# Kernel tuning notes

Measured on AMD Instinct MI355X. Metric: run time of the kernel, lower is better.

The kernel has to match this reference:

```python
import jax, jax.numpy as jnp
import numpy as np

B = 8192; L = 50; D_EMB = 128
N_USER = 100000; N_MOVIE = 50000; N_DENSE = 8
D = 2 * D_EMB + D_EMB + N_DENSE  # 392 total_input_dim
E = 4; T = 2; H1 = 256; H2 = 128; ATT_H = 64; N_CROSS = 3


def setup_inputs() -> dict:
    key = jax.random.key(0)
    ks = jax.random.split(key, 28)
    rn = lambda k, shape, s=0.02: jax.random.normal(k, shape, jnp.float32) * s
    inp = {
        'userId': jax.random.randint(ks[0], (B,), 0, N_USER),
        'movieId': jax.random.randint(ks[1], (B,), 0, N_MOVIE),
        'seq_history': jax.random.randint(ks[2], (B, L), 0, N_MOVIE),
        'dense_feats': jax.random.normal(ks[3], (B, N_DENSE), jnp.float32),
        # embeddings (row 0 is padding_idx -> zeros)
        'emb_user': rn(ks[4], (N_USER + 1, D_EMB)).at[0].set(0.0),
        'emb_movie': rn(ks[5], (N_MOVIE + 1, D_EMB)).at[0].set(0.0),
        # DIN attention MLP: input [q,k,q-k,q*k] = 4*D_EMB
        'att_w1': rn(ks[6], (4 * D_EMB, ATT_H)), 'att_b1': jnp.zeros((ATT_H,), jnp.float32),
        'att_w2': rn(ks[7], (ATT_H, 1)), 'att_b2': jnp.zeros((1,), jnp.float32),
        # LayerNorms
        'in_gamma': jnp.ones((D,), jnp.float32), 'in_beta': jnp.zeros((D,), jnp.float32),
        'cr_gamma': jnp.ones((D,), jnp.float32), 'cr_beta': jnp.zeros((D,), jnp.float32),
        # CrossNetV2: x_{l+1} = x0 * (x_l W_l + b_l) + x_l
        'cross_W': rn(ks[8], (N_CROSS, D, D)), 'cross_b': jnp.zeros((N_CROSS, D), jnp.float32),
        # MMoE experts: Linear(D,H1)-ReLU-Linear(H1,H2), batched over E
        'exp_w1': rn(ks[9], (E, D, H1)), 'exp_b1': jnp.zeros((E, H1), jnp.float32),
        'exp_w2': rn(ks[10], (E, H1, H2)), 'exp_b2': jnp.zeros((E, H2), jnp.float32),
        # gates per task
        'gate_w': rn(ks[11], (T, D, E)), 'gate_b': jnp.zeros((T, E), jnp.float32),
        # task heads Linear(H2, 1)
        'head_w': rn(ks[12], (T, H2)), 'head_b': jnp.zeros((T,), jnp.float32),
    }
    return inp


def _layernorm(x, g, b, eps=1e-5):
    m = jnp.mean(x, axis=-1, keepdims=True)
    v = jnp.var(x, axis=-1, keepdims=True)
    return (x - m) * jax.lax.rsqrt(v + eps) * g + b


def _forward(userId, movieId, seq_history, dense_feats, emb_user, emb_movie,
             att_w1, att_b1, att_w2, att_b2, in_gamma, in_beta,
             cross_W, cross_b, cr_gamma, cr_beta,
             exp_w1, exp_b1, exp_w2, exp_b2, gate_w, gate_b, head_w, head_b):
    # sparse embedding gathers
    user_e = emb_user[userId]            # [B, D_EMB]
    movie_e = emb_movie[movieId]         # [B, D_EMB]  (target item)
    hist = emb_movie[seq_history]        # [B, L, D_EMB]
    mask = seq_history > 0               # [B, L]

    # DIN attention pooling
    q = jnp.broadcast_to(movie_e[:, None, :], hist.shape)            # [B, L, D_EMB]
    att_in = jnp.concatenate([q, hist, q - hist, q * hist], axis=-1)  # [B, L, 4*D_EMB]
    scores = (jax.nn.relu(att_in @ att_w1 + att_b1) @ att_w2 + att_b2)[..., 0]  # [B, L]
    scores = jnp.where(mask, scores, -1e9)
    probs = jax.nn.softmax(scores, axis=-1)                           # [B, L]
    interest = jnp.einsum('bl,bld->bd', probs, hist)                  # [B, D_EMB]

    x = jnp.concatenate([user_e, movie_e, interest, dense_feats], axis=-1)  # [B, D]
    x = _layernorm(x, in_gamma, in_beta)

    # CrossNetV2
    x0 = x
    for l in range(N_CROSS):
        x = x0 * (x @ cross_W[l] + cross_b[l]) + x
    x = _layernorm(x, cr_gamma, cr_beta)

    # MMoE: batched expert GEMMs + per-task soft gates
    h = jax.nn.relu(jnp.einsum('bd,edh->ebh', x, exp_w1) + exp_b1[:, None, :])  # [E,B,H1]
    eo = jnp.einsum('ebh,eho->ebo', h, exp_w2) + exp_b2[:, None, :]             # [E,B,H2]
    g = jax.nn.softmax(jnp.einsum('bd,tde->tbe', x, gate_w) + gate_b[:, None, :], axis=-1)  # [T,B,E]
    task_feat = jnp.einsum('tbe,ebo->tbo', g, eo)                                # [T,B,H2]

    logits = jnp.einsum('tbo,to->tb', task_feat, head_w) + head_b[:, None]       # [T,B]
    return logits


def reference(userId, movieId, seq_history, dense_feats, emb_user, emb_movie,
              att_w1, att_b1, att_w2, att_b2, in_gamma, in_beta,
              cross_W, cross_b, cr_gamma, cr_beta,
              exp_w1, exp_b1, exp_w2, exp_b2, gate_w, gate_b, head_w, head_b):
    return _forward(userId, movieId, seq_history, dense_feats, emb_user, emb_movie,
                    att_w1, att_b1, att_w2, att_b2, in_gamma, in_beta,
                    cross_W, cross_b, cr_gamma, cr_beta,
                    exp_w1, exp_b1, exp_w2, exp_b2, gate_w, gate_b, head_w, head_b)
```

## Files before the change

### kernel.cpp

```cpp
#include <hip/hip_runtime.h>
#include <hip/hip_bf16.h>

typedef short short8 __attribute__((ext_vector_type(8)));
typedef short short4v __attribute__((ext_vector_type(4)));
typedef float f32x4 __attribute__((ext_vector_type(4)));

constexpr int BB = 8192;
constexpr int LL = 50;
constexpr int DE = 128;
constexpr int DD = 392;
constexpr int HH1 = 256;
constexpr int HH2 = 128;

__device__ __forceinline__ short f2b(float x) {
    __hip_bfloat16 h = __float2bfloat16(x);
    return __builtin_bit_cast(short, h);
}
__device__ __forceinline__ float b2f(short v) {
    unsigned u = ((unsigned)(unsigned short)v) << 16;
    return __builtin_bit_cast(float, u);
}

__global__ __launch_bounds__(256) void prep_small(
    const float* __restrict__ w1,
    const float* __restrict__ w2, const float* __restrict__ b2,
    const float* __restrict__ head_w,
    short* __restrict__ Wqpb, short* __restrict__ WkFb, short* __restrict__ WpFb,
    float* __restrict__ hw2, float* __restrict__ hc)
{
    __shared__ float hw[256];
    const int b = blockIdx.x, t = threadIdx.x;
    if (b < 32) {
        int idx = b * 256 + t;
        Wqpb[idx] = f2b(w1[idx] + w1[idx + 16384]);
    } else if (b < 64) {
        int o = (b - 32) * 256 + t;
        int e = o & 7, lane = (o >> 3) & 63, nt = (o >> 9) & 3, kt = o >> 11;
        int k = (kt << 5) + ((lane >> 4) << 3) + e;
        int h = (nt << 4) + (lane & 15);
        WkFb[o] = f2b(w1[(128 + k) * 64 + h] - w1[(256 + k) * 64 + h]);
        WpFb[o] = f2b(w1[(384 + k) * 64 + h]);
    } else {
        const int e = b - 64;
        hw[t] = head_w[t];
        __syncthreads();
        const float* row = &w2[((long)e * HH1 + t) * HH2];
        float s0 = 0.f, s1 = 0.f;
        #pragma unroll 8
        for (int o = 0; o < 128; o += 4) {
            float4 v = *reinterpret_cast<const float4*>(&row[o]);
            s0 += v.x * hw[o] + v.y * hw[o + 1] + v.z * hw[o + 2] + v.w * hw[o + 3];
            s1 += v.x * hw[128 + o] + v.y * hw[129 + o] + v.z * hw[130 + o] + v.w * hw[131 + o];
        }
        hw2[(((e << 8) + t) << 1) + 0] = s0;
        hw2[(((e << 8) + t) << 1) + 1] = s1;
        if (t < 2) {
            float s = 0.f;
            for (int o = 0; o < 128; ++o) s += b2[e * 128 + o] * hw[t * 128 + o];
            hc[e * 2 + t] = s;
        }
    }
}

constexpr int S0 = 3 * 392 * 392;
constexpr int S1 = 4 * 392 * 256;
constexpr int S2 = (50001 * 128) / 4;

__global__ __launch_bounds__(256) void prep_trans(
    const float* __restrict__ cross_W, const float* __restrict__ exp_w1,
    const float* __restrict__ emb_movie,
    short* __restrict__ WTc, short* __restrict__ WT1, short* __restrict__ embB)
{
    int idx = blockIdx.x * 256 + threadIdx.x;
    if (idx < S0) {
        int z = idx / (392 * 392), rr = idx - z * 392 * 392;
        int c = rr / 392, r = rr - c * 392;
        WTc[idx] = f2b(cross_W[(long)z * 153664 + r * 392 + c]);
    } else if (idx < S0 + S1) {
        int j = idx - S0;
        int z = j / 100352, rr = j - z * 100352;
        int c = rr / 392, r = rr - c * 392;
        WT1[j] = f2b(exp_w1[(long)z * 100352 + r * 256 + c]);
    } else if (idx < S0 + S1 + S2) {
        long j = (long)(idx - S0 - S1) << 2;
        float4 v = *reinterpret_cast<const float4*>(&emb_movie[j]);
        short4v o;
        o[0] = f2b(v.x); o[1] = f2b(v.y); o[2] = f2b(v.z); o[3] = f2b(v.w);
        *reinterpret_cast<short4v*>(&embB[j]) = o;
    }
}

__global__ __launch_bounds__(256, 8) void attn_kernel(
    const int* __restrict__ userId, const int* __restrict__ movieId,
    const int* __restrict__ seq, const float* __restrict__ dense,
    const float* __restrict__ emb_user, const float* __restrict__ emb_movie,
    const short* __restrict__ embB,
    const short* __restrict__ Wqpb, const short* __restrict__ WkFb,
    const short* __restrict__ WpFb,
    const float* __restrict__ att_b1, const float* __restrict__ att_w2,
    const float* __restrict__ att_b2,
    const float* __restrict__ in_gamma, const float* __restrict__ in_beta,
    float* __restrict__ x0f, short* __restrict__ x0b)
{
    __shared__ short hist[64 * 128];
    __shared__ float qs[128];
    __shared__ int   seq_s[64];
    __shared__ float qconst[64];
    __shared__ float sp[4][64];
    __shared__ float probs[64];
    __shared__ float xrow[392];
    __shared__ float stats[2];

    const int b = blockIdx.x;
    const int t = threadIdx.x;
    const int lane = t & 63;
    const int w = t >> 6;

    if (t < 128) qs[t] = emb_movie[(long)movieId[b] * DE + t];
    if (t < 64)  seq_s[t] = (t < LL) ? seq[b * LL + t] : 0;
    __syncthreads();

    #pragma unroll
    for (int i = 0; i < 4; ++i) {
        const int idx = t + (i << 8);
        const int l = idx >> 4, c = idx & 15;
        short8 hv = *reinterpret_cast<const short8*>(&embB[(long)seq_s[l] * DE + (c << 3)]);
        const int byte = (l << 8) + ((c << 4) ^ ((l & 7) << 4));
        *reinterpret_cast<short8*>(reinterpret_cast<char*>(hist) + byte) = hv;
    }

    float ue = (t < 128) ? emb_user[(long)userId[b] * DE + t] : 0.f;
    float dv = (t < 8) ? dense[b * 8 + t] : 0.f;

    short8 bfrag[4];
    #pragma unroll
    for (int kt = 0; kt < 4; ++kt) {
        const int fo = ((((kt << 2) + w) << 6) | lane) << 3;
        short8 wk = *reinterpret_cast<const short8*>(&WkFb[fo]);
        short8 wp = *reinterpret_cast<const short8*>(&WpFb[fo]);
        const int kq = (kt << 5) + ((lane >> 4) << 3);
        #pragma unroll
        for (int j = 0; j < 8; ++j)
            bfrag[kt][j] = f2b(fmaf(qs[kq + j], b2f(wp[j]), b2f(wk[j])));
    }

    {
        float s = 0.f;
        const int dq = w << 5;
        #pragma unroll
        for (int dd = 0; dd < 32; ++dd)
            s = fmaf(qs[dq + dd], b2f(Wqpb[(dq + dd) * 64 + lane]), s);
        sp[w][lane] = s;
    }
    __syncthreads();
    if (t < 64) qconst[t] = att_b1[t] + sp[0][t] + sp[1][t] + sp[2][t] + sp[3][t];
    __syncthreads();

    {
        const float qc  = qconst[(w << 4) + (lane & 15)];
        const float w2v = att_w2[(w << 4) + (lane & 15)];
        #pragma unroll
        for (int mt = 0; mt < 4; ++mt) {
            f32x4 acc;
            #pragma unroll
            for (int r = 0; r < 4; ++r) acc[r] = qc;
            const int row = (mt << 4) + (lane & 15);
            const int rbase = row << 8;
            const int swz = (row & 7) << 4;
            #pragma unroll
            for (int kt = 0; kt < 4; ++kt) {
                const int kbyte = (kt << 6) + ((lane >> 4) << 4);
                short8 a = *reinterpret_cast<const short8*>(
                    reinterpret_cast<char*>(hist) + rbase + (kbyte ^ swz));
                acc = __builtin_amdgcn_mfma_f32_16x16x32_bf16(a, bfrag[kt], acc, 0, 0, 0);
            }
            #pragma unroll
            for (int r = 0; r < 4; ++r) {
                float v = fmaxf(acc[r], 0.f) * w2v;
                v += __shfl_xor(v, 1); v += __shfl_xor(v, 2);
                v += __shfl_xor(v, 4); v += __shfl_xor(v, 8);
                if ((lane & 15) == 0)
                    sp[w][(mt << 4) + ((lane >> 4) << 2) + r] = v;
            }
        }
    }
    __syncthreads();

    if (t < 64) {
        float sc = sp[0][t] + sp[1][t] + sp[2][t] + sp[3][t] + att_b2[0];
        float s = (t < LL) ? ((seq_s[t] > 0) ? sc : -1e9f) : -INFINITY;
        float m = s;
        #pragma unroll
        for (int off = 32; off > 0; off >>= 1) m = fmaxf(m, __shfl_xor(m, off));
        float e = (t < LL) ? __expf(s - m) : 0.f;
        float sum = e;
        #pragma unroll
        for (int off = 32; off > 0; off >>= 1) sum += __shfl_xor(sum, off);
        probs[t] = (t < LL) ? (e / sum) : 0.f;
    }
    __syncthreads();

    const int g  = t >> 5;
    const int d0 = (t & 31) << 2;
    float4 ps = make_float4(0.f, 0.f, 0.f, 0.f);
    #pragma unroll
    for (int i = 0; i < 8; ++i) {
        const int l = g + (i << 3);
        const int byte = (l << 8) + ((d0 << 1) ^ ((l & 7) << 4));
        short4v hv = *reinterpret_cast<const short4v*>(
            reinterpret_cast<const char*>(hist) + byte);
        const float p = probs[l];
        ps.x = fmaf(p, b2f(hv[0]), ps.x);
        ps.y = fmaf(p, b2f(hv[1]), ps.y);
        ps.z = fmaf(p, b2f(hv[2]), ps.z);
        ps.w = fmaf(p, b2f(hv[3]), ps.w);
    }
    ps.x += __shfl_xor(ps.x, 32); ps.y += __shfl_xor(ps.y, 32);
    ps.z += __shfl_xor(ps.z, 32); ps.w += __shfl_xor(ps.w, 32);
    __syncthreads();
    float* scr = reinterpret_cast<float*>(hist);
    if (lane < 32)
        *reinterpret_cast<float4*>(&scr[(w << 7) + ((lane & 31) << 2)]) = ps;
    __syncthreads();
    if (t < 128) {
        xrow[256 + t] = scr[t] + scr[128 + t] + scr[256 + t] + scr[384 + t];
        xrow[t] = ue;
        xrow[128 + t] = qs[t];
        if (t < 8) xrow[384 + t] = dv;
    }
    __syncthreads();

    float v0 = xrow[t];
    float v1 = (t < 136) ? xrow[256 + t] : 0.f;
    float s2 = v0 + v1, q2 = v0 * v0 + v1 * v1;
    #pragma unroll
    for (int off = 32; off > 0; off >>= 1) {
        s2 += __shfl_xor(s2, off);
        q2 += __shfl_xor(q2, off);
    }
    if (lane == 0) { sp[0][w] = s2; sp[1][w] = q2; }
    __syncthreads();
    if (t == 0) {
        float S = sp[0][0] + sp[0][1] + sp[0][2] + sp[0][3];
        float Q = sp[1][0] + sp[1][1] + sp[1][2] + sp[1][3];
        float mean = S / (float)DD;
        float var = Q / (float)DD - mean * mean;
        stats[0] = mean;
        stats[1] = rsqrtf(var + 1e-5f);
    }
    __syncthreads();
    const float mean = stats[0], inv = stats[1];
    const long base = (long)b * DD;
    float o0 = (v0 - mean) * inv * in_gamma[t] + in_beta[t];
    x0f[base + t] = o0; x0b[base + t] = f2b(o0);
    if (t < 136) {
        float o1 = (v1 - mean) * inv * in_gamma[256 + t] + in_beta[256 + t];
        x0f[base + 256 + t] = o1; x0b[base + 256 + t] = f2b(o1);
    }
}

template<int MODE, int WF32, int WB16, int NXB, int NZB>
__global__ __launch_bounds__(256) void bgemm(
    const short* __restrict__ A, const short* __restrict__ WT,
    const float* __restrict__ bias,
    float* __restrict__ outF, short* __restrict__ outB,
    const float* __restrict__ x0, const float* __restrict__ xin,
    int M, int N, int K, long aZ, long wZ, long bZ, long oZ)
{
    __shared__ short As[2][64 * 64];
    __shared__ short Bs[2][64 * 64];

    int id = blockIdx.x;
    const int qq = (int)gridDim.x >> 3;
    id = (id & 7) * qq + (id >> 3);
    const int mb  = id / (NXB * NZB);
    const int rem = id - mb * (NXB * NZB);
    const int z   = rem / NXB;
    const int xb  = rem - z * NXB;

    A += (long)z * aZ; WT += (long)z * wZ; bias += (long)z * bZ;
    const long oz = (long)z * oZ;

    const int t = threadIdx.x, w = t >> 6, lane = t & 63;
    const int m0 = mb * 64, n0 = xb * 64;
    const int sm = t >> 3, sk8 = (t & 7) << 3;

    f32x4 acc[4];
    #pragma unroll
    for (int i = 0; i < 4; ++i) {
        #pragma unroll
        for (int r = 0; r < 4; ++r) acc[i][r] = 0.f;
    }

    const int nsteps = (K + 63) >> 6;
    short8 avr[2], bvr[2];

    auto loadr = [&](int k0) {
        #pragma unroll
        for (int i = 0; i < 2; ++i) {
            const int r = sm + (i << 5);
            short8 zv = {0, 0, 0, 0, 0, 0, 0, 0};
            avr[i] = zv; bvr[i] = zv;
            if (k0 + sk8 < K) {
                avr[i] = *reinterpret_cast<const short8*>(&A[(long)(m0 + r) * K + k0 + sk8]);
                if (n0 + r < N)
                    bvr[i] = *reinterpret_cast<const short8*>(&WT[(long)(n0 + r) * K + k0 + sk8]);
            }
        }
    };
    auto writelds = [&](int buf) {
        #pragma unroll
        for (int i = 0; i < 2; ++i) {
            const int r = sm + (i << 5);
            const int byte = (r << 7) + ((sk8 << 1) ^ ((r & 7) << 4));
            *reinterpret_cast<short8*>(reinterpret_cast<char*>(&As[buf][0]) + byte) = avr[i];
            *reinterpret_cast<short8*>(reinterpret_cast<char*>(&Bs[buf][0]) + byte) = bvr[i];
        }
    };

    loadr(0);
    writelds(0);
    __syncthreads();

    int cur = 0;
    for (int s = 0; s < nsteps; ++s) {
        if (s + 1 < nsteps) loadr((s + 1) << 6);
        #pragma unroll
        for (int kt = 0; kt < 2; ++kt) {
            const int kbyte = (kt << 6) + ((lane >> 4) << 4);
            const int ar = (w << 4) + (lane & 15);
            short8 a = *reinterpret_cast<const short8*>(
                reinterpret_cast<char*>(&As[cur][0]) + (ar << 7) + (kbyte ^ ((ar & 7) << 4)));
            #pragma unroll
            for (int nt = 0; nt < 4; ++nt) {
                const int br = (nt << 4) + (lane & 15);
                short8 bb = *reinterpret_cast<const short8*>(
                    reinterpret_cast<char*>(&Bs[cur][0]) + (br << 7) + (kbyte ^ ((br & 7) << 4)));
                acc[nt] = __builtin_amdgcn_mfma_f32_16x16x32_bf16(a, bb, acc[nt], 0, 0, 0);
            }
        }
        if (s + 1 < nsteps) writelds(cur ^ 1);
        __syncthreads();
        cur ^= 1;
    }

    #pragma unroll
    for (int nt = 0; nt < 4; ++nt) {
        const int col = n0 + (nt << 4) + (lane & 15);
        if (col < N) {
            const float bv = bias[col];
            #pragma unroll
            for (int r = 0; r < 4; ++r) {
                const int row = m0 + (w << 4) + ((lane >> 4) << 2) + r;
                float v = acc[nt][r] + bv;
                if (MODE == 1) v = fmaxf(v, 0.f);
                const long o = (long)row * N + col;
                if (MODE == 2) v = x0[o] * v + xin[o];
                if (WF32) outF[oz + o] = v;
                if (WB16) outB[oz + o] = f2b(v);
            }
        }
    }
}

__global__ __launch_bounds__(256) void ln_kernel(
    const float* __restrict__ in,
    const float* __restrict__ gamma, const float* __restrict__ beta,
    float* __restrict__ outF, short* __restrict__ outB)
{
    __shared__ float red[2][4];
    __shared__ float stats[2];
    const int b = blockIdx.x, t = threadIdx.x, lane = t & 63, w = t >> 6;
    const long base = (long)b * DD;
    float v0 = in[base + t];
    float v1 = (t < 136) ? in[base + 256 + t] : 0.f;
    float s = v0 + v1, q2 = v0 * v0 + v1 * v1;
    #pragma unroll
    for (int off = 32; off > 0; off >>= 1) {
        s += __shfl_xor(s, off);
        q2 += __shfl_xor(q2, off);
    }
    if (lane == 0) { red[0][w] = s; red[1][w] = q2; }
    __syncthreads();
    if (t == 0) {
        float S = red[0][0] + red[0][1] + red[0][2] + red[0][3];
        float Q = red[1][0] + red[1][1] + red[1][2] + red[1][3];
        float mean = S / (float)DD;
        float var = Q / (float)DD - mean * mean;
        stats[0] = mean;
        stats[1] = rsqrtf(var + 1e-5f);
    }
    __syncthreads();
    const float mean = stats[0], inv = stats[1];
    float o0 = (v0 - mean) * inv * gamma[t] + beta[t];
    outF[base + t] = o0; outB[base + t] = f2b(o0);
    if (t < 136) {
        float o1 = (v1 - mean) * inv * gamma[256 + t] + beta[256 + t];
        outF[base + 256 + t] = o1; outB[base + 256 + t] = f2b(o1);
    }
}

__global__ __launch_bounds__(256) void final_kernel(
    const float* __restrict__ x, const short* __restrict__ h1,
    const float* __restrict__ hw2, const float* __restrict__ hc,
    const float* __restrict__ gate_w, const float* __restrict__ gate_b,
    const float* __restrict__ head_b, float* __restrict__ out)
{
    const int t = threadIdx.x, lane = t & 63, w = t >> 6;
    const int b = blockIdx.x * 4 + w;
    const float* xr = x + (long)b * DD;

    float xv[7];
    #pragma unroll
    for (int i = 0; i < 7; ++i) {
        int d = lane + (i << 6);
        xv[i] = (d < DD) ? xr[d] : 0.f;
    }

    float gl[8] = {0.f, 0.f, 0.f, 0.f, 0.f, 0.f, 0.f, 0.f};
    #pragma unroll
    for (int i = 0; i < 7; ++i) {
        int d = lane + (i << 6);
        if (d < DD) {
            float4 g0 = *reinterpret_cast<const float4*>(&gate_w[d << 2]);
            float4 g1 = *reinterpret_cast<const float4*>(&gate_w[1568 + (d << 2)]);
            gl[0] = fmaf(xv[i], g0.x, gl[0]); gl[1] = fmaf(xv[i], g0.y, gl[1]);
            gl[2] = fmaf(xv[i], g0.z, gl[2]); gl[3] = fmaf(xv[i], g0.w, gl[3]);
            gl[4] = fmaf(xv[i], g1.x, gl[4]); gl[5] = fmaf(xv[i], g1.y, gl[5]);
            gl[6] = fmaf(xv[i], g1.z, gl[6]); gl[7] = fmaf(xv[i], g1.w, gl[7]);
        }
    }

    float ed[8];
    #pragma unroll
    for (int e = 0; e < 4; ++e) {
        short4v hv = *reinterpret_cast<const short4v*>(
            &h1[((long)e * BB + b) * HH1 + (lane << 2)]);
        const float* hwp = &hw2[(((e << 8) + (lane << 2))) << 1];
        float4 w01 = *reinterpret_cast<const float4*>(hwp);
        float4 w23 = *reinterpret_cast<const float4*>(hwp + 4);
        float h0 = b2f(hv[0]), h1f = b2f(hv[1]), h2 = b2f(hv[2]), h3 = b2f(hv[3]);
        ed[e]     = fmaf(h0, w01.x, fmaf(h1f, w01.z, fmaf(h2, w23.x, h3 * w23.z)));
        ed[4 + e] = fmaf(h0, w01.y, fmaf(h1f, w01.w, fmaf(h2, w23.y, h3 * w23.w)));
    }

    #pragma unroll
    for (int v = 0; v < 8; ++v) {
        #pragma unroll
        for (int off = 32; off > 0; off >>= 1) {
            gl[v] += __shfl_xor(gl[v], off);
            ed[v] += __shfl_xor(ed[v], off);
        }
    }

    if (lane == 0) {
        float res[2];
        #pragma unroll
        for (int tt = 0; tt < 2; ++tt) {
            float lv[4], m = -1e30f;
            #pragma unroll
            for (int e = 0; e < 4; ++e) {
                lv[e] = gl[tt * 4 + e] + gate_b[tt * 4 + e];
                m = fmaxf(m, lv[e]);
            }
            float sum = 0.f, acc = 0.f;
            #pragma unroll
            for (int e = 0; e < 4; ++e) { lv[e] = __expf(lv[e] - m); sum += lv[e]; }
            #pragma unroll
            for (int e = 0; e < 4; ++e)
                acc = fmaf(lv[e], ed[tt * 4 + e] + hc[e * 2 + tt], acc);
            res[tt] = head_b[tt] + acc / sum;
        }
        out[b] = res[0];
        out[BB + b] = res[1];
    }
}

extern "C" void kernel_launch(void* const* d_in, const int* in_sizes, int n_in,
                              void* d_out, int out_size, void* d_ws, size_t ws_size,
                              hipStream_t stream) {
    const int*   userId    = (const int*)d_in[0];
    const int*   movieId   = (const int*)d_in[1];
    const int*   seq       = (const int*)d_in[2];
    const float* dense     = (const float*)d_in[3];
    const float* emb_user  = (const float*)d_in[4];
    const float* emb_movie = (const float*)d_in[5];
    const float* att_w1    = (const float*)d_in[6];
    const float* att_b1    = (const float*)d_in[7];
    const float* att_w2    = (const float*)d_in[8];
    const float* att_b2    = (const float*)d_in[9];
    const float* in_gamma  = (const float*)d_in[10];
    const float* in_beta   = (const float*)d_in[11];
    const float* cr_gamma  = (const float*)d_in[12];
    const float* cr_beta   = (const float*)d_in[13];
    const float* cross_W   = (const float*)d_in[14];
    const float* cross_b   = (const float*)d_in[15];
    const float* exp_w1    = (const float*)d_in[16];
    const float* exp_b1    = (const float*)d_in[17];
    const float* exp_w2    = (const float*)d_in[18];
    const float* exp_b2    = (const float*)d_in[19];
    const float* gate_w    = (const float*)d_in[20];
    const float* gate_b    = (const float*)d_in[21];
    const float* head_w    = (const float*)d_in[22];
    const float* head_b    = (const float*)d_in[23];
    float* outp = (float*)d_out;

    char* p = (char*)d_ws;
    auto alloc = [&](size_t bytes) -> char* {
        char* r = p; p += (bytes + 255) & ~(size_t)255; return r;
    };
    short* Wqpb = (short*)alloc(8192 * 2);
    short* WkFb = (short*)alloc(8192 * 2);
    short* WpFb = (short*)alloc(8192 * 2);
    float* hw2 = (float*)alloc(2048 * 4);
    float* hc  = (float*)alloc(8 * 4);
    short* WTc = (short*)alloc((size_t)3 * 392 * 392 * 2);
    short* WT1 = (short*)alloc((size_t)4 * 256 * 392 * 2);
    short* embB = (short*)alloc((size_t)50001 * 128 * 2);
    float* x0f = (float*)alloc((size_t)BB * DD * 4);
    short* x0b = (short*)alloc((size_t)BB * DD * 2);
    float* xAf = (float*)alloc((size_t)BB * DD * 4);
    short* xAb = (short*)alloc((size_t)BB * DD * 2);
    float* xBf = (float*)alloc((size_t)BB * DD * 4);
    short* xBb = (short*)alloc((size_t)BB * DD * 2);
    short* h1b = (short*)alloc((size_t)4 * BB * HH1 * 2);

    prep_small<<<68, 256, 0, stream>>>(att_w1, exp_w2, exp_b2, head_w,
                                       Wqpb, WkFb, WpFb, hw2, hc);
    prep_trans<<<(S0 + S1 + S2 + 255) / 256, 256, 0, stream>>>(
        cross_W, exp_w1, emb_movie, WTc, WT1, embB);

    attn_kernel<<<BB, 256, 0, stream>>>(userId, movieId, seq, dense,
                                        emb_user, emb_movie, embB,
                                        Wqpb, WkFb, WpFb,
                                        att_b1, att_w2, att_b2,
                                        in_gamma, in_beta, x0f, x0b);

    bgemm<2, 1, 1, 7, 1><<<896, 256, 0, stream>>>(x0b, WTc, cross_b, xAf, xAb,
                                                  x0f, x0f, BB, DD, DD, 0, 0, 0, 0);
    bgemm<2, 1, 1, 7, 1><<<896, 256, 0, stream>>>(xAb, WTc + 392 * 392, cross_b + 392,
                                                  xBf, xBb, x0f, xAf, BB, DD, DD, 0, 0, 0, 0);
    bgemm<2, 1, 0, 7, 1><<<896, 256, 0, stream>>>(xBb, WTc + 2 * 392 * 392, cross_b + 784,
                                                  xAf, nullptr, x0f, xBf, BB, DD, DD, 0, 0, 0, 0);

    ln_kernel<<<BB, 256, 0, stream>>>(xAf, cr_gamma, cr_beta, xBf, xBb);

    bgemm<1, 0, 1, 4, 4><<<2048, 256, 0, stream>>>(
        xBb, WT1, exp_b1, nullptr, h1b, nullptr, nullptr,
        BB, HH1, DD, 0, (long)HH1 * DD, HH1, (long)BB * HH1);

    final_kernel<<<BB / 4, 256, 0, stream>>>(xBf, h1b, hw2, hc,
                                             gate_w, gate_b, head_b, outp);

    (void)in_sizes; (void)n_in; (void)out_size; (void)ws_size;
}
```

Baseline: 175.1 us.

## Deepen bgemm global prefetch and trim attention-kernel barriers and weight layouts

The bgemm main loop now keeps two register staging sets so global loads are issued two K-steps ahead of the MFMA work, hiding more memory latency at the cost of extra VGPRs. In the attention kernel, the query-projection weights are transposed so each thread reads them as vector loads, and the key and product weight fragments are interleaved into one buffer. The per-column query constant is now computed per thread instead of in a separate shared-memory step, and the row-assembly shared buffer is removed, dropping several __syncthreads. Higher register pressure in bgemm could reduce occupancy.

New measurement: 174.3 us. About the same (-0.4%).

```diff
diff --git a/kernel.cpp b/kernel.cpp
--- a/kernel.cpp
+++ b/kernel.cpp
@@ -25,21 +25,23 @@
     const float* __restrict__ w1,
     const float* __restrict__ w2, const float* __restrict__ b2,
     const float* __restrict__ head_w,
-    short* __restrict__ Wqpb, short* __restrict__ WkFb, short* __restrict__ WpFb,
+    short* __restrict__ WqpT, short* __restrict__ WkpF,
     float* __restrict__ hw2, float* __restrict__ hc)
 {
     __shared__ float hw[256];
     const int b = blockIdx.x, t = threadIdx.x;
     if (b < 32) {
-        int idx = b * 256 + t;
-        Wqpb[idx] = f2b(w1[idx] + w1[idx + 16384]);
+        int o = b * 256 + t;
+        int h = o >> 7, d = o & 127;
+        WqpT[o] = f2b(w1[d * 64 + h] + w1[16384 + d * 64 + h]);
     } else if (b < 64) {
         int o = (b - 32) * 256 + t;
         int e = o & 7, lane = (o >> 3) & 63, nt = (o >> 9) & 3, kt = o >> 11;
         int k = (kt << 5) + ((lane >> 4) << 3) + e;
         int h = (nt << 4) + (lane & 15);
-        WkFb[o] = f2b(w1[(128 + k) * 64 + h] - w1[(256 + k) * 64 + h]);
-        WpFb[o] = f2b(w1[(384 + k) * 64 + h]);
+        int base = (o >> 3) << 4;
+        WkpF[base + e]     = f2b(w1[(128 + k) * 64 + h] - w1[(256 + k) * 64 + h]);
+        WkpF[base + 8 + e] = f2b(w1[(384 + k) * 64 + h]);
     } else {
         const int e = b - 64;
         hw[t] = head_w[t];
@@ -95,8 +97,7 @@
     const int* __restrict__ seq, const float* __restrict__ dense,
     const float* __restrict__ emb_user, const float* __restrict__ emb_movie,
     const short* __restrict__ embB,
-    const short* __restrict__ Wqpb, const short* __restrict__ WkFb,
-    const short* __restrict__ WpFb,
+    const short* __restrict__ WqpT, const short* __restrict__ WkpF,
     const float* __restrict__ att_b1, const float* __restrict__ att_w2,
     const float* __restrict__ att_b2,
     const float* __restrict__ in_gamma, const float* __restrict__ in_beta,
@@ -105,10 +106,10 @@
     __shared__ short hist[64 * 128];
     __shared__ float qs[128];
     __shared__ int   seq_s[64];
-    __shared__ float qconst[64];
     __shared__ float sp[4][64];
+    __shared__ float spS[4][64];
     __shared__ float probs[64];
-    __shared__ float xrow[392];
+    __shared__ float ibuf[4][128];
     __shared__ float stats[2];
 
     const int b = blockIdx.x;
@@ -130,14 +131,14 @@
     }
 
     float ue = (t < 128) ? emb_user[(long)userId[b] * DE + t] : 0.f;
-    float dv = (t < 8) ? dense[b * 8 + t] : 0.f;
+    float dv = (t >= 128 && t < 136) ? dense[b * 8 + (t - 128)] : 0.f;
 
     short8 bfrag[4];
     #pragma unroll
     for (int kt = 0; kt < 4; ++kt) {
-        const int fo = ((((kt << 2) + w) << 6) | lane) << 3;
-        short8 wk = *reinterpret_cast<const short8*>(&WkFb[fo]);
-        short8 wp = *reinterpret_cast<const short8*>(&WpFb[fo]);
+        const int fo = ((((kt << 2) + w) << 6) | lane) << 4;
+        short8 wk = *reinterpret_cast<const short8*>(&WkpF[fo]);
+        short8 wp = *reinterpret_cast<const short8*>(&WkpF[fo + 8]);
         const int kq = (kt << 5) + ((lane >> 4) << 3);
         #pragma unroll
         for (int j = 0; j < 8; ++j)
@@ -146,24 +147,25 @@
 
     {
         float s = 0.f;
-        const int dq = w << 5;
-        #pragma unroll
-        for (int dd = 0; dd < 32; ++dd)
-            s = fmaf(qs[dq + dd], b2f(Wqpb[(dq + dd) * 64 + lane]), s);
+        const short* wq = &WqpT[(lane << 7) + (w << 5)];
+        #pragma unroll
+        for (int c = 0; c < 4; ++c) {
+            short8 wv = *reinterpret_cast<const short8*>(&wq[c << 3]);
+            #pragma unroll
+            for (int j = 0; j < 8; ++j)
+                s = fmaf(qs[(w << 5) + (c << 3) + j], b2f(wv[j]), s);
+        }
         sp[w][lane] = s;
     }
     __syncthreads();
-    if (t < 64) qconst[t] = att_b1[t] + sp[0][t] + sp[1][t] + sp[2][t] + sp[3][t];
-    __syncthreads();
 
     {
-        const float qc  = qconst[(w << 4) + (lane & 15)];
-        const float w2v = att_w2[(w << 4) + (lane & 15)];
+        const int col = (w << 4) + (lane & 15);
+        const float qc = att_b1[col] + sp[0][col] + sp[1][col] + sp[2][col] + sp[3][col];
+        const float w2v = att_w2[col];
         #pragma unroll
         for (int mt = 0; mt < 4; ++mt) {
-            f32x4 acc;
-            #pragma unroll
-            for (int r = 0; r < 4; ++r) acc[r] = qc;
+            f32x4 acc = {0.f, 0.f, 0.f, 0.f};
             const int row = (mt << 4) + (lane & 15);
             const int rbase = row << 8;
             const int swz = (row & 7) << 4;
@@ -176,18 +178,18 @@
             }
             #pragma unroll
             for (int r = 0; r < 4; ++r) {
-                float v = fmaxf(acc[r], 0.f) * w2v;
+                float v = fmaxf(acc[r] + qc, 0.f) * w2v;
                 v += __shfl_xor(v, 1); v += __shfl_xor(v, 2);
                 v += __shfl_xor(v, 4); v += __shfl_xor(v, 8);
                 if ((lane & 15) == 0)
-                    sp[w][(mt << 4) + ((lane >> 4) << 2) + r] = v;
+                    spS[w][(mt << 4) + ((lane >> 4) << 2) + r] = v;
             }
         }
     }
     __syncthreads();
 
     if (t < 64) {
-        float sc = sp[0][t] + sp[1][t] + sp[2][t] + sp[3][t] + att_b2[0];
+        float sc = spS[0][t] + spS[1][t] + spS[2][t] + spS[3][t] + att_b2[0];
         float s = (t < LL) ? ((seq_s[t] > 0) ? sc : -1e9f) : -INFINITY;
         float m = s;
         #pragma unroll
@@ -217,21 +219,15 @@
     }
     ps.x += __shfl_xor(ps.x, 32); ps.y += __shfl_xor(ps.y, 32);
     ps.z += __shfl_xor(ps.z, 32); ps.w += __shfl_xor(ps.w, 32);
-    __syncthreads();
-    float* scr = reinterpret_cast<float*>(hist);
     if (lane < 32)
-        *reinterpret_cast<float4*>(&scr[(w << 7) + ((lane & 31) << 2)]) = ps;
-    __syncthreads();
-    if (t < 128) {
-        xrow[256 + t] = scr[t] + scr[128 + t] + scr[256 + t] + scr[384 + t];
-        xrow[t] = ue;
-        xrow[128 + t] = qs[t];
-        if (t < 8) xrow[384 + t] = dv;
-    }
-    __syncthreads();
-
-    float v0 = xrow[t];
-    float v1 = (t < 136) ? xrow[256 + t] : 0.f;
+        *reinterpret_cast<float4*>(&ibuf[w][lane << 2]) = ps;
+    __syncthreads();
+
+    float v0 = (t < 128) ? ue : qs[t - 128];
+    float v1 = 0.f;
+    if (t < 128)       v1 = ibuf[0][t] + ibuf[1][t] + ibuf[2][t] + ibuf[3][t];
+    else if (t < 136)  v1 = dv;
+
     float s2 = v0 + v1, q2 = v0 * v0 + v1 * v1;
     #pragma unroll
     for (int off = 32; off > 0; off >>= 1) {
@@ -293,56 +289,89 @@
     }
 
     const int nsteps = (K + 63) >> 6;
-    short8 avr[2], bvr[2];
-
-    auto loadr = [&](int k0) {
+    short8 avA[2], bvA[2], avB[2], bvB[2];
+
+    auto loadA = [&](int k0) {
         #pragma unroll
         for (int i = 0; i < 2; ++i) {
             const int r = sm + (i << 5);
             short8 zv = {0, 0, 0, 0, 0, 0, 0, 0};
-            avr[i] = zv; bvr[i] = zv;
+            avA[i] = zv; bvA[i] = zv;
             if (k0 + sk8 < K) {
-                avr[i] = *reinterpret_cast<const short8*>(&A[(long)(m0 + r) * K + k0 + sk8]);
+                avA[i] = *reinterpret_cast<const short8*>(&A[(long)(m0 + r) * K + k0 + sk8]);
                 if (n0 + r < N)
-                    bvr[i] = *reinterpret_cast<const short8*>(&WT[(long)(n0 + r) * K + k0 + sk8]);
+                    bvA[i] = *reinterpret_cast<const short8*>(&WT[(long)(n0 + r) * K + k0 + sk8]);
             }
         }
     };
-    auto writelds = [&](int buf) {
+    auto loadB = [&](int k0) {
+        #pragma unroll
+        for (int i = 0; i < 2; ++i) {
+            const int r = sm + (i << 5);
+            short8 zv = {0, 0, 0, 0, 0, 0, 0, 0};
+            avB[i] = zv; bvB[i] = zv;
+            if (k0 + sk8 < K) {
+                avB[i] = *reinterpret_cast<const short8*>(&A[(long)(m0 + r) * K + k0 + sk8]);
+                if (n0 + r < N)
+                    bvB[i] = *reinterpret_cast<const short8*>(&WT[(long)(n0 + r) * K + k0 + sk8]);
+            }
+        }
+    };
+    auto wrA = [&](int buf) {
         #pragma unroll
         for (int i = 0; i < 2; ++i) {
             const int r = sm + (i << 5);
             const int byte = (r << 7) + ((sk8 << 1) ^ ((r & 7) << 4));
-            *reinterpret_cast<short8*>(reinterpret_cast<char*>(&As[buf][0]) + byte) = avr[i];
-            *reinterpret_cast<short8*>(reinterpret_cast<char*>(&Bs[buf][0]) + byte) = bvr[i];
+            *reinterpret_cast<short8*>(reinterpret_cast<char*>(&As[buf][0]) + byte) = avA[i];
+            *reinterpret_cast<short8*>(reinterpret_cast<char*>(&Bs[buf][0]) + byte) = bvA[i];
         }
     };
-
-    loadr(0);
-    writelds(0);
-    __syncthreads();
-
-    int cur = 0;
-    for (int s = 0; s < nsteps; ++s) {
-        if (s + 1 < nsteps) loadr((s + 1) << 6);
+    auto wrB = [&](int buf) {
+        #pragma unroll
+        for (int i = 0; i < 2; ++i) {
+            const int r = sm + (i << 5);
+            const int byte = (r << 7) + ((sk8 << 1) ^ ((r & 7) << 4));
+            *reinterpret_cast<short8*>(reinterpret_cast<char*>(&As[buf][0]) + byte) = avB[i];
+            *reinterpret_cast<short8*>(reinterpret_cast<char*>(&Bs[buf][0]) + byte) = bvB[i];
+        }
+    };
+    auto domfma = [&](int buf) {
         #pragma unroll
         for (int kt = 0; kt < 2; ++kt) {
             const int kbyte = (kt << 6) + ((lane >> 4) << 4);
             const int ar = (w << 4) + (lane & 15);
             short8 a = *reinterpret_cast<const short8*>(
-                reinterpret_cast<char*>(&As[cur][0]) + (ar << 7) + (kbyte ^ ((ar & 7) << 4)));
+                reinterpret_cast<char*>(&As[buf][0]) + (ar << 7) + (kbyte ^ ((ar & 7) << 4)));
             #pragma unroll
             for (int nt = 0; nt < 4; ++nt) {
                 const int br = (nt << 4) + (lane & 15);
                 short8 bb = *reinterpret_cast<const short8*>(
-                    reinterpret_cast<char*>(&Bs[cur][0]) + (br << 7) + (kbyte ^ ((br & 7) << 4)));
+                    reinterpret_cast<char*>(&Bs[buf][0]) + (br << 7) + (kbyte ^ ((br & 7) << 4)));
                 acc[nt] = __builtin_amdgcn_mfma_f32_16x16x32_bf16(a, bb, acc[nt], 0, 0, 0);
             }
         }
-        if (s + 1 < nsteps) writelds(cur ^ 1);
-        __syncthreads();
-        cur ^= 1;
-    }
+    };
+
+    loadA(0);
+    wrA(0);
+    if (nsteps > 1) loadA(64);
+    if (nsteps > 2) loadB(128);
+    __syncthreads();
+
+    int cur = 0, s = 0;
+    while (s + 1 < nsteps) {
+        domfma(cur);
+        wrA(cur ^ 1);
+        if (s + 3 < nsteps) loadA((s + 3) << 6);
+        __syncthreads(); cur ^= 1; ++s;
+        if (s + 1 < nsteps) {
+            domfma(cur);
+            wrB(cur ^ 1);
+            if (s + 3 < nsteps) loadB((s + 3) << 6);
+            __syncthreads(); cur ^= 1; ++s;
+        }
+    }
+    domfma(cur);
 
     #pragma unroll
     for (int nt = 0; nt < 4; ++nt) {
@@ -509,9 +538,8 @@
     auto alloc = [&](size_t bytes) -> char* {
         char* r = p; p += (bytes + 255) & ~(size_t)255; return r;
     };
-    short* Wqpb = (short*)alloc(8192 * 2);
-    short* WkFb = (short*)alloc(8192 * 2);
-    short* WpFb = (short*)alloc(8192 * 2);
+    short* WqpT = (short*)alloc(8192 * 2);
+    short* WkpF = (short*)alloc(16384 * 2);
     float* hw2 = (float*)alloc(2048 * 4);
     float* hc  = (float*)alloc(8 * 4);
     short* WTc = (short*)alloc((size_t)3 * 392 * 392 * 2);
@@ -526,13 +554,13 @@
     short* h1b = (short*)alloc((size_t)4 * BB * HH1 * 2);
 
     prep_small<<<68, 256, 0, stream>>>(att_w1, exp_w2, exp_b2, head_w,
-                                       Wqpb, WkFb, WpFb, hw2, hc);
+                                       WqpT, WkpF, hw2, hc);
     prep_trans<<<(S0 + S1 + S2 + 255) / 256, 256, 0, stream>>>(
         cross_W, exp_w1, emb_movie, WTc, WT1, embB);
 
     attn_kernel<<<BB, 256, 0, stream>>>(userId, movieId, seq, dense,
                                         emb_user, emb_movie, embB,
-                                        Wqpb, WkFb, WpFb,
+                                        WqpT, WkpF,
                                         att_b1, att_w2, att_b2,
                                         in_gamma, in_beta, x0f, x0b);
 
```
